# Kernel optimization log

Measured on AMD Instinct MI355X. Metric: run time of the kernel, lower is better.

The kernel has to match this reference:

```python
import jax, jax.numpy as jnp
import numpy as np
from math import ceil

B, T, FQ, D = 2, 48, 100, 512
H, DFF, L, WSZ = 8, 2048, 6, 8


def setup_inputs() -> dict:
    key = jax.random.key(0)
    ks = jax.random.split(key, 8)
    g = lambda k, shape: jax.random.normal(k, shape, jnp.float32) * 0.02
    return {
        "frame_queries": jax.random.normal(ks[0], (B, T, FQ, D), jnp.float32),
        "Wp": g(ks[1], (D, D)), "bp": jnp.zeros((D,), jnp.float32),
        "Wqkv": g(ks[2], (L, 3 * D, D)), "bqkv": jnp.zeros((L, 3 * D), jnp.float32),
        "Wo": g(ks[3], (L, D, D)), "bo": jnp.zeros((L, D), jnp.float32),
        "ln1_s": jnp.ones((L, D), jnp.float32), "ln1_b": jnp.zeros((L, D), jnp.float32),
        "W1": g(ks[4], (L, DFF, D)), "b1": jnp.zeros((L, DFF), jnp.float32),
        "W2": g(ks[5], (L, D, DFF)), "b2": jnp.zeros((L, D), jnp.float32),
        "ln2_s": jnp.ones((L, D), jnp.float32), "ln2_b": jnp.zeros((L, D), jnp.float32),
    }


def _ln(x, s, b, eps=1e-5):
    mu = x.mean(-1, keepdims=True)
    var = ((x - mu) ** 2).mean(-1, keepdims=True)
    return (x - mu) * jax.lax.rsqrt(var + eps) * s + b


def _mha(x, Wqkv_i, bqkv_i, Wo_i, bo_i, add_mask):
    # x: [Bw, S, C]; add_mask: None or [Bw, 1, S, S] additive float
    Bw, S, C = x.shape
    hd = C // H
    qkv = x @ Wqkv_i.T + bqkv_i
    q, k, v = jnp.split(qkv, 3, axis=-1)
    q = q.reshape(Bw, S, H, hd).transpose(0, 2, 1, 3)
    k = k.reshape(Bw, S, H, hd).transpose(0, 2, 1, 3)
    v = v.reshape(Bw, S, H, hd).transpose(0, 2, 1, 3)
    scores = jnp.einsum('bhqd,bhkd->bhqk', q, k) * jnp.float32(1.0 / np.sqrt(hd))
    if add_mask is not None:
        scores = scores + add_mask
    a = jax.nn.softmax(scores, axis=-1)
    o = jnp.einsum('bhqk,bhkd->bhqd', a, v).transpose(0, 2, 1, 3).reshape(Bw, S, C)
    return o @ Wo_i.T + bo_i


def _shift_mask():
    # padding mask is all-False (T % WSZ == 0), faithful construction of the
    # shifted-window additive mask as in the torch code.
    Nw = T // WSZ
    half = int(ceil(WSZ / 2))
    S = WSZ * FQ
    am = jnp.zeros((B, T), dtype=bool)
    r = jnp.roll(am, half, axis=1).reshape(B, Nw, WSZ)
    m = jnp.broadcast_to(r[..., None], (B, Nw, WSZ, WSZ))
    m = m.at[:, 0].set(m[:, 0] | m[:, 0].swapaxes(-1, -2))
    m = m.at[:, -1].set(m[:, -1] | m[:, -1].swapaxes(-1, -2))
    m = m.at[:, 0, :half, half:].set(True)
    m = m.at[:, 0, half:, :half].set(True)
    mfull = jnp.broadcast_to(m.reshape(B * Nw, WSZ, 1, WSZ, 1),
                             (B * Nw, WSZ, FQ, WSZ, FQ)).reshape(B * Nw, S, S)
    return (mfull.astype(jnp.float32) * -1000.0)[:, None]  # [B*Nw,1,S,S]


def reference(frame_queries, Wp, bp, Wqkv, bqkv, Wo, bo, ln1_s, ln1_b,
              W1, b1, W2, b2, ln2_s, ln2_b):
    Nw = T // WSZ
    half = int(ceil(WSZ / 2))
    S = WSZ * FQ
    x = frame_queries @ Wp.T + bp  # [B, T, FQ, D]
    shift_add = _shift_mask()
    for i in range(L):
        if i % 2 == 0:
            # plain window attention
            xw = x.reshape(B * Nw, S, D)
            xw = _ln(xw + _mha(xw, Wqkv[i], bqkv[i], Wo[i], bo[i], None),
                     ln1_s[i], ln1_b[i])
            x = xw.reshape(B, T, FQ, D)
        else:
            # shifted window attention
            xs = jnp.roll(x, half, axis=1)
            xw = xs.reshape(B * Nw, S, D)
            xw = _ln(xw + _mha(xw, Wqkv[i], bqkv[i], Wo[i], bo[i], shift_add),
                     ln1_s[i], ln1_b[i])
            x = jnp.roll(xw.reshape(B, T, FQ, D), -half, axis=1)
        # FFN (pointwise over channel dim)
        h = jax.nn.relu(x @ W1[i].T + b1[i]) @ W2[i].T + b2[i]
        x = _ln(x + h, ln2_s[i], ln2_b[i])
    return x  # [B, T, FQ, D] == 'lb t nq c'
```

## Files before the change

### kernel.cpp

```cpp
#include <hip/hip_runtime.h>


typedef float  f4    __attribute__((ext_vector_type(4)));
typedef __bf16 bf8   __attribute__((ext_vector_type(8)));
typedef unsigned short u16x8 __attribute__((ext_vector_type(8)));
typedef unsigned short u16x4 __attribute__((ext_vector_type(4)));

__device__ __forceinline__ unsigned short f2bf(float f) {
    unsigned int u = __builtin_bit_cast(unsigned int, f);
    u += 0x7fffu + ((u >> 16) & 1u);
    return (unsigned short)(u >> 16);
}
__device__ __forceinline__ float bf2f(unsigned short s) {
    return __builtin_bit_cast(float, ((unsigned int)s) << 16);
}

#define GLD16(gp, lp) __builtin_amdgcn_global_load_lds( \
    (const __attribute__((address_space(1))) void*)(gp), \
    (__attribute__((address_space(3))) void*)(lp), 16, 0, 0)

__device__ __forceinline__ int map_row(int r, int rshift) {
    if (!rshift) return r;
    int bb = r / 4800, rem = r % 4800;
    int tt = rem / 100, f = rem - tt * 100;
    return bb * 4800 + ((tt + rshift) % 48) * 100 + f;
}

template<int BM>
__global__ __launch_bounds__(256) void mfma_gemm(
    const unsigned short* __restrict__ A, const unsigned short* __restrict__ W,
    const float* __restrict__ bias, float* Cf, unsigned short* Cb,
    int M, int N, int K, int relu, int rshift, int qscale, int NB)
{
    constexpr int MI      = BM / 32;
    constexpr int ABUF    = BM * 32;
    constexpr int SB      = ABUF + 4096;
    constexpr int AROUNDS = BM / 64;
    __shared__ unsigned short Ls[3 * SB];
    const int tid = threadIdx.x, lane = tid & 63, wave = tid >> 6;

    const int per = gridDim.x >> 3;
    const int l = (blockIdx.x & 7) * per + (blockIdx.x >> 3);
    const int MB = M / BM;
    if (l >= NB * MB) return;
    const int n0 = (l % NB) * 128, m0 = (l / NB) * BM;

    const unsigned short* ga[AROUNDS];
    #pragma unroll
    for (int it = 0; it < AROUNDS; ++it) {
        int s = it * 256 + tid, row = s >> 2, cg = (s & 3) ^ ((row >> 1) & 3);
        ga[it] = A + (size_t)map_row(m0 + row, rshift) * K + cg * 8;
    }
    const unsigned short* gb[2];
    #pragma unroll
    for (int it = 0; it < 2; ++it) {
        int s = it * 256 + tid, row = s >> 2, cg = (s & 3) ^ ((row >> 1) & 3);
        gb[it] = W + (size_t)(n0 + row) * K + cg * 8;
    }

    const int wm = (wave >> 1) * (BM / 2), wn = (wave & 1) * 64;
    const int lr = lane & 15, quad = lane >> 4;

    auto STAGE = [&](int kt2, int buf) {
        const int k1 = kt2 << 5;
        unsigned short* Lb = &Ls[buf * SB];
        #pragma unroll
        for (int it = 0; it < AROUNDS; ++it)
            GLD16(ga[it] + k1, &Lb[(it * 256 + wave * 64) * 8]);
        #pragma unroll
        for (int it = 0; it < 2; ++it)
            GLD16(gb[it] + k1, &Lb[ABUF + (it * 256 + wave * 64) * 8]);
    };

    f4 acc[MI][4];
    #pragma unroll
    for (int i = 0; i < MI; ++i)
        #pragma unroll
        for (int j = 0; j < 4; ++j) acc[i][j] = 0.f;

    const int NK = K >> 5;
    STAGE(0, 0);
    STAGE(1, 1);

    int cb = 0;
    for (int kt = 0; kt < NK; ++kt) {
        if (kt + 1 < NK) {
            if constexpr (BM == 128) asm volatile("s_waitcnt vmcnt(4)" ::: "memory");
            else                     asm volatile("s_waitcnt vmcnt(3)" ::: "memory");
        } else {
            asm volatile("s_waitcnt vmcnt(0)" ::: "memory");
        }
        __builtin_amdgcn_s_barrier();
        __builtin_amdgcn_sched_barrier(0);
        const int ib = (cb == 0) ? 2 : cb - 1;
        if (kt + 2 < NK) STAGE(kt + 2, ib);

        const unsigned short* Ab = &Ls[cb * SB];
        const unsigned short* Bb = &Ls[cb * SB + ABUF];
        bf8 af[MI], bfr[4];
        #pragma unroll
        for (int mi = 0; mi < MI; ++mi) {
            int m = wm + mi * 16 + lr;
            int c = quad ^ ((m >> 1) & 3);
            af[mi] = __builtin_bit_cast(bf8, *(const u16x8*)&Ab[(m * 4 + c) * 8]);
        }
        #pragma unroll
        for (int ni = 0; ni < 4; ++ni) {
            int n = wn + ni * 16 + lr;
            int c = quad ^ ((n >> 1) & 3);
            bfr[ni] = __builtin_bit_cast(bf8, *(const u16x8*)&Bb[(n * 4 + c) * 8]);
        }
        #pragma unroll
        for (int mi = 0; mi < MI; ++mi)
            #pragma unroll
            for (int ni = 0; ni < 4; ++ni)
                acc[mi][ni] = __builtin_amdgcn_mfma_f32_16x16x32_bf16(
                    af[mi], bfr[ni], acc[mi][ni], 0, 0, 0);
        __builtin_amdgcn_sched_barrier(0);
        cb = (cb + 1 == 3) ? 0 : cb + 1;
    }

    #pragma unroll
    for (int mi = 0; mi < MI; ++mi) {
        #pragma unroll
        for (int ni = 0; ni < 4; ++ni) {
            const int rowg = m0 + wm + mi * 16 + quad * 4;
            const int colg = n0 + wn + ni * 16 + lr;
            const float bv = bias[colg];
            const float sc = (qscale && colg < 512) ? 0.125f : 1.0f;
            #pragma unroll
            for (int r = 0; r < 4; ++r) {
                float v = (acc[mi][ni][r] + bv) * sc;
                if (relu) v = fmaxf(v, 0.f);
                const size_t off = (size_t)(rowg + r) * N + colg;
                if (Cf) Cf[off] = v;
                if (Cb) Cb[off] = f2bf(v);
            }
        }
    }
}

template<int BM>
__global__ __launch_bounds__(256) void gemm_bk64(
    const unsigned short* __restrict__ A, const unsigned short* __restrict__ W,
    const float* __restrict__ bias, float* Cf, unsigned short* Cb,
    int M, int N, int K, int relu, int rshift, int qscale)
{
    constexpr int MI      = BM / 32;
    constexpr int ABUF    = BM * 64;
    constexpr int AROUNDS = BM / 32;
    __shared__ unsigned short As[2 * ABUF];
    __shared__ unsigned short Bs[2 * 8192];
    const int tid = threadIdx.x, lane = tid & 63, wave = tid >> 6;
    const int n0 = blockIdx.x * 128, m0 = blockIdx.y * BM;

    const unsigned short* ga[AROUNDS];
    unsigned short* la[AROUNDS];
    #pragma unroll
    for (int it = 0; it < AROUNDS; ++it) {
        int s = it * 256 + tid, row = s >> 3, cg = (s & 7) ^ (row & 7);
        ga[it] = A + (size_t)map_row(m0 + row, rshift) * K + cg * 8;
        la[it] = &As[(it * 256 + wave * 64) * 8];
    }
    const unsigned short* gb[4];
    unsigned short* lb[4];
    #pragma unroll
    for (int it = 0; it < 4; ++it) {
        int s = it * 256 + tid, row = s >> 3, cg = (s & 7) ^ (row & 7);
        gb[it] = W + (size_t)(n0 + row) * K + cg * 8;
        lb[it] = &Bs[(it * 256 + wave * 64) * 8];
    }

    const int wm = (wave >> 1) * (BM / 2), wn = (wave & 1) * 64;
    const int lr = lane & 15, quad = lane >> 4;

    f4 acc[MI][4];
    #pragma unroll
    for (int i = 0; i < MI; ++i)
        #pragma unroll
        for (int j = 0; j < 4; ++j) acc[i][j] = 0.f;

    #pragma unroll
    for (int it = 0; it < AROUNDS; ++it) GLD16(ga[it], la[it]);
    #pragma unroll
    for (int it = 0; it < 4; ++it) GLD16(gb[it], lb[it]);

    const int NK = K >> 6;
    for (int kt = 0; kt < NK; ++kt) {
        const int cb = kt & 1, nb = cb ^ 1;
        __syncthreads();
        if (kt + 1 < NK) {
            const int k1 = (kt + 1) << 6;
            #pragma unroll
            for (int it = 0; it < AROUNDS; ++it) GLD16(ga[it] + k1, la[it] + nb * ABUF);
            #pragma unroll
            for (int it = 0; it < 4; ++it)       GLD16(gb[it] + k1, lb[it] + nb * 8192);
        }
        const unsigned short* Ab = &As[cb * ABUF];
        const unsigned short* Bb = &Bs[cb * 8192];
        #pragma unroll
        for (int kh = 0; kh < 2; ++kh) {
            bf8 af[MI], bfr[4];
            #pragma unroll
            for (int mi = 0; mi < MI; ++mi) {
                int m = wm + mi * 16 + lr;
                int c = (kh * 4 + quad) ^ (m & 7);
                af[mi] = __builtin_bit_cast(bf8, *(const u16x8*)&Ab[(m * 8 + c) * 8]);
            }
            #pragma unroll
            for (int ni = 0; ni < 4; ++ni) {
                int n = wn + ni * 16 + lr;
                int c = (kh * 4 + quad) ^ (n & 7);
                bfr[ni] = __builtin_bit_cast(bf8, *(const u16x8*)&Bb[(n * 8 + c) * 8]);
            }
            #pragma unroll
            for (int mi = 0; mi < MI; ++mi)
                #pragma unroll
                for (int ni = 0; ni < 4; ++ni)
                    acc[mi][ni] = __builtin_amdgcn_mfma_f32_16x16x32_bf16(
                        af[mi], bfr[ni], acc[mi][ni], 0, 0, 0);
        }
    }

    #pragma unroll
    for (int mi = 0; mi < MI; ++mi) {
        #pragma unroll
        for (int ni = 0; ni < 4; ++ni) {
            const int rowg = m0 + wm + mi * 16 + quad * 4;
            const int colg = n0 + wn + ni * 16 + lr;
            const float bv = bias[colg];
            const float sc = (qscale && colg < 512) ? 0.125f : 1.0f;
            #pragma unroll
            for (int r = 0; r < 4; ++r) {
                float v = (acc[mi][ni][r] + bv) * sc;
                if (relu) v = fmaxf(v, 0.f);
                const size_t off = (size_t)(rowg + r) * N + colg;
                if (Cf) Cf[off] = v;
                if (Cb) Cb[off] = f2bf(v);
            }
        }
    }
}

__global__ __launch_bounds__(320) void flash_attn_mfma(
    const unsigned short* __restrict__ qkv, unsigned short* __restrict__ o,
    int masked)
{
    __shared__ unsigned short Ks[2][2048];
    __shared__ unsigned short VT[2][64 * 34];
    __shared__ unsigned short Ps[5][576];

    const int bid = blockIdx.x;
    const int h = bid & 7, kk2 = bid >> 3;
    const int qt = kk2 % 10, w = kk2 / 10;
    const int tid = threadIdx.x, lane = tid & 63, wave = tid >> 6;
    const int lr = lane & 15, quad = lane >> 4;
    const int qb = qt * 80 + wave * 16;
    const size_t wbase = (size_t)w * 800 * 1536;
    const bool do_mask = masked && ((w % 6) == 0);

    bf8 aQ[2];
    {
        const unsigned short* qp =
            qkv + wbase + (size_t)(qb + lr) * 1536 + h * 64 + quad * 8;
        aQ[0] = __builtin_bit_cast(bf8, *(const u16x8*)qp);
        aQ[1] = __builtin_bit_cast(bf8, *(const u16x8*)(qp + 32));
    }

    const unsigned short* gk = qkv;
    int kw = 0;
    if (wave < 4) {
        int s = wave * 64 + lane, row = s >> 3, clog = (s & 7) ^ (row & 7);
        gk = qkv + wbase + (size_t)row * 1536 + 512 + h * 64 + clog * 8;
        kw = wave * 512;
    }
    const int vkey = tid >> 3, vd0 = (tid & 7) * 8;
    const unsigned short* gv =
        qkv + wbase + (size_t)vkey * 1536 + 1024 + h * 64 + vd0;

    float lsum = 0.f;
    f4 oacc[4];
    #pragma unroll
    for (int dt = 0; dt < 4; ++dt) oacc[dt] = 0.f;

    const bool qhl = (qb + lr) >= 400;

    if (wave < 4) GLD16(gk, &Ks[0][kw]);
    if (tid < 256) {
        u16x8 vv0 = *(const u16x8*)gv;
        #pragma unroll
        for (int j = 0; j < 8; ++j) VT[0][(vd0 + j) * 34 + vkey] = vv0[j];
    }

    for (int kt = 0; kt < 25; ++kt) {
        const int cb = kt & 1, nb = cb ^ 1;
        const int k0 = kt * 32;
        __syncthreads();

        u16x8 vv;
        const bool pf = (kt < 24);
        if (pf && wave < 4) GLD16(gk + (size_t)(k0 + 32) * 1536, &Ks[nb][kw]);
        if (pf && tid < 256) vv = *(const u16x8*)(gv + (size_t)(k0 + 32) * 1536);

        f4 st[2];
        st[0] = 0.f; st[1] = 0.f;
        __builtin_amdgcn_s_setprio(1);
        #pragma unroll
        for (int kh = 0; kh < 2; ++kh) {
            const int cx = (kh * 4 + quad) ^ (lane & 7);
            bf8 kf0 = __builtin_bit_cast(bf8, *(const u16x8*)&Ks[cb][(lr * 8 + cx) * 8]);
            bf8 kf1 = __builtin_bit_cast(bf8, *(const u16x8*)&Ks[cb][((16 + lr) * 8 + cx) * 8]);
            st[0] = __builtin_amdgcn_mfma_f32_16x16x32_bf16(kf0, aQ[kh], st[0], 0, 0, 0);
            st[1] = __builtin_amdgcn_mfma_f32_16x16x32_bf16(kf1, aQ[kh], st[1], 0, 0, 0);
        }
        __builtin_amdgcn_s_setprio(0);

        {
            u16x4 pk0, pk1;
            float ls = 0.f;
            #pragma unroll
            for (int r = 0; r < 4; ++r) {
                float a = st[0][r], b = st[1][r];
                if (do_mask) {
                    if (((k0 + quad * 4 + r) >= 400) != qhl)      a -= 1000.f;
                    if (((k0 + 16 + quad * 4 + r) >= 400) != qhl) b -= 1000.f;
                }
                float p0 = __expf(fminf(a, 80.f));
                float p1 = __expf(fminf(b, 80.f));
                ls += p0 + p1;
                pk0[r] = (unsigned short)(__builtin_bit_cast(unsigned int, p0) >> 16);
                pk1[r] = (unsigned short)(__builtin_bit_cast(unsigned int, p1) >> 16);
            }
            lsum += ls;
            *(u16x4*)&Ps[wave][lr * 36 + quad * 4]      = pk0;
            *(u16x4*)&Ps[wave][lr * 36 + 16 + quad * 4] = pk1;
        }

        if (pf && tid < 256) {
            #pragma unroll
            for (int j = 0; j < 8; ++j) VT[nb][(vd0 + j) * 34 + vkey] = vv[j];
        }

        bf8 aP = __builtin_bit_cast(bf8, *(const u16x8*)&Ps[wave][lr * 36 + quad * 8]);
        __builtin_amdgcn_s_setprio(1);
        #pragma unroll
        for (int dt = 0; dt < 4; ++dt) {
            bf8 bV = __builtin_bit_cast(bf8,
                *(const u16x8*)&VT[cb][(dt * 16 + lr) * 34 + quad * 8]);
            oacc[dt] = __builtin_amdgcn_mfma_f32_16x16x32_bf16(aP, bV, oacc[dt], 0, 0, 0);
        }
        __builtin_amdgcn_s_setprio(0);
    }

    {
        float l = lsum;
        l += __shfl_xor(l, 16);
        l += __shfl_xor(l, 32);
        float inv[4];
        #pragma unroll
        for (int r = 0; r < 4; ++r)
            inv[r] = 1.0f / __shfl(l, quad * 4 + r);
        #pragma unroll
        for (int dt = 0; dt < 4; ++dt)
            #pragma unroll
            for (int r = 0; r < 4; ++r)
                o[((size_t)w * 800 + qb + quad * 4 + r) * 512 + h * 64 + dt * 16 + lr] =
                    f2bf(oacc[dt][r] * inv[r]);
    }
}

__global__ __launch_bounds__(256) void add_ln_kernel(
    const unsigned short* xb, const unsigned short* dlt,
    const float* __restrict__ s, const float* __restrict__ b,
    float* outf, unsigned short* outb, int rshift)
{
    const int wave = threadIdx.x >> 6, lane = threadIdx.x & 63;
    const int row = blockIdx.x * 4 + wave;
    const int xrow = map_row(row, rshift);
    const int c = lane * 8;
    u16x8 xv = *(const u16x8*)(xb  + (size_t)xrow * 512 + c);
    u16x8 dv = *(const u16x8*)(dlt + (size_t)row  * 512 + c);
    f4 u0, u1;
    #pragma unroll
    for (int j = 0; j < 4; ++j) {
        u0[j] = bf2f(xv[j])     + bf2f(dv[j]);
        u1[j] = bf2f(xv[4 + j]) + bf2f(dv[4 + j]);
    }
    float sum = u0[0]+u0[1]+u0[2]+u0[3] + u1[0]+u1[1]+u1[2]+u1[3];
    #pragma unroll
    for (int o2 = 1; o2 < 64; o2 <<= 1) sum += __shfl_xor(sum, o2);
    const float mu = sum * (1.0f / 512.0f);
    f4 d0 = u0 - mu, d1 = u1 - mu;
    float sq = d0[0]*d0[0]+d0[1]*d0[1]+d0[2]*d0[2]+d0[3]*d0[3]
             + d1[0]*d1[0]+d1[1]*d1[1]+d1[2]*d1[2]+d1[3]*d1[3];
    #pragma unroll
    for (int o2 = 1; o2 < 64; o2 <<= 1) sq += __shfl_xor(sq, o2);
    const float rs = rsqrtf(sq * (1.0f / 512.0f) + 1e-5f);
    f4 s0 = *(const f4*)(s + c), s1 = *(const f4*)(s + c + 4);
    f4 b0 = *(const f4*)(b + c), b1 = *(const f4*)(b + c + 4);
    f4 y0, y1;
    #pragma unroll
    for (int j = 0; j < 4; ++j) { y0[j] = d0[j]*rs*s0[j]+b0[j]; y1[j] = d1[j]*rs*s1[j]+b1[j]; }
    u16x8 ob;
    #pragma unroll
    for (int j = 0; j < 4; ++j) { ob[j] = f2bf(y0[j]); ob[4+j] = f2bf(y1[j]); }
    *(u16x8*)(outb + (size_t)xrow * 512 + c) = ob;
    if (outf) {
        float* of = outf + (size_t)xrow * 512 + c;
        *(f4*)of = y0; *(f4*)(of + 4) = y1;
    }
}

__global__ __launch_bounds__(256) void cast_f2b_kernel(
    const float* __restrict__ in, unsigned short* __restrict__ out, int n4)
{
    const int i = blockIdx.x * 256 + threadIdx.x;
    if (i >= n4) return;
    f4 v = ((const f4*)in)[i];
    u16x4 o4 = {f2bf(v[0]), f2bf(v[1]), f2bf(v[2]), f2bf(v[3])};
    ((u16x4*)out)[i] = o4;
}

extern "C" void kernel_launch(void* const* d_in, const int* in_sizes, int n_in,
                              void* d_out, int out_size, void* d_ws, size_t ws_size,
                              hipStream_t stream)
{
    const float* fq   = (const float*)d_in[0];
    const float* Wp   = (const float*)d_in[1];
    const float* bp   = (const float*)d_in[2];
    const float* Wqkv = (const float*)d_in[3];
    const float* bqkv = (const float*)d_in[4];
    const float* Wo   = (const float*)d_in[5];
    const float* bo   = (const float*)d_in[6];
    const float* l1s  = (const float*)d_in[7];
    const float* l1b  = (const float*)d_in[8];
    const float* W1   = (const float*)d_in[9];
    const float* b1   = (const float*)d_in[10];
    const float* W2   = (const float*)d_in[11];
    const float* b2   = (const float*)d_in[12];
    const float* l2s  = (const float*)d_in[13];
    const float* l2b  = (const float*)d_in[14];
    float* out = (float*)d_out;

    unsigned short* xb   = (unsigned short*)d_ws;
    unsigned short* qkvb = xb + 4915200;
    unsigned short* hbuf = qkvb + 14745600;
    unsigned short* wbuf = hbuf + 19660800;
    unsigned short* obuf = hbuf;
    unsigned short* t1b  = qkvb;
    unsigned short* fqb  = hbuf;
    unsigned short* wqA = wbuf;
    unsigned short* woA = wqA + 4718592;
    unsigned short* w1A = woA + 1572864;
    unsigned short* w2A = w1A + 6291456;
    unsigned short* wpA = w2A + 6291456;

    const dim3 blk(256);
    #define G8(n) dim3((((n) + 7) & ~7))
    cast_f2b_kernel<<<dim3(4800), blk, 0, stream>>>(fq,   fqb, 1228800);
    cast_f2b_kernel<<<dim3(4608), blk, 0, stream>>>(Wqkv, wqA, 1179648);
    cast_f2b_kernel<<<dim3(1536), blk, 0, stream>>>(Wo,   woA, 393216);
    cast_f2b_kernel<<<dim3(6144), blk, 0, stream>>>(W1,   w1A, 1572864);
    cast_f2b_kernel<<<dim3(6144), blk, 0, stream>>>(W2,   w2A, 1572864);
    cast_f2b_kernel<<<dim3(256),  blk, 0, stream>>>(Wp,   wpA, 65536);
    mfma_gemm<64><<<G8(600), blk, 0, stream>>>(fqb, wpA, bp, nullptr, xb,
                                               9600, 512, 512, 0, 0, 0, 4);

    for (int i = 0; i < 6; ++i) {
        const int rsh = (i & 1) ? 44 : 0;
        const unsigned short* wq = wqA + (size_t)i * 786432;
        const unsigned short* wo = woA + (size_t)i * 262144;
        const unsigned short* w1 = w1A + (size_t)i * 1048576;
        const unsigned short* w2 = w2A + (size_t)i * 1048576;
        mfma_gemm<128><<<G8(900), blk, 0, stream>>>(xb, wq, bqkv + i * 1536,
                                                    nullptr, qkvb, 9600, 1536, 512, 0, rsh, 1, 12);
        flash_attn_mfma<<<dim3(960), dim3(320), 0, stream>>>(qkvb, obuf, i & 1);
        mfma_gemm<64><<<G8(600), blk, 0, stream>>>(obuf, wo, bo + i * 512,
                                                   nullptr, t1b, 9600, 512, 512, 0, 0, 0, 4);
        add_ln_kernel<<<dim3(2400), blk, 0, stream>>>(xb, t1b, l1s + i * 512, l1b + i * 512,
                                                      nullptr, xb, rsh);
        gemm_bk64<128><<<dim3(16, 75), blk, 0, stream>>>(xb, w1, b1 + i * 2048,
                                                         nullptr, hbuf, 9600, 2048, 512, 1, 0, 0);
        gemm_bk64<64><<<dim3(4, 150), blk, 0, stream>>>(hbuf, w2, b2 + i * 512,
                                                        nullptr, t1b, 9600, 512, 2048, 0, 0, 0);
        add_ln_kernel<<<dim3(2400), blk, 0, stream>>>(xb, t1b, l2s + i * 512, l2b + i * 512,
                                                      (i == 5) ? out : nullptr, xb, 0);
    }
    #undef G8
}
```

Baseline: 1.191 ms.

## Load V tiles via async global-to-LDS and transpose with ds_read_b64_tr_b16

Replaces the register-staged V load and scalar transposed LDS stores with direct global_load_lds copies into a permuted layout. The B operand is then read with the hardware transposing LDS read instruction. This removes per-element 2-byte LDS stores and the register round trip on the V path, so the V prefetch overlaps with compute the same way K does. It relies on a hand-derived key/dim permutation and inline asm with an explicit waitcnt, which limits compiler scheduling and is fragile if the layout mapping is wrong.

```diff
diff --git a/kernel.cpp b/kernel.cpp
--- a/kernel.cpp
+++ b/kernel.cpp
@@ -5,6 +5,8 @@
 typedef __bf16 bf8   __attribute__((ext_vector_type(8)));
 typedef unsigned short u16x8 __attribute__((ext_vector_type(8)));
 typedef unsigned short u16x4 __attribute__((ext_vector_type(4)));
+typedef unsigned int   u32x2 __attribute__((ext_vector_type(2)));
+typedef unsigned int   u32x4 __attribute__((ext_vector_type(4)));
 
 __device__ __forceinline__ unsigned short f2bf(float f) {
     unsigned int u = __builtin_bit_cast(unsigned int, f);
@@ -247,7 +249,7 @@
     int masked)
 {
     __shared__ unsigned short Ks[2][2048];
-    __shared__ unsigned short VT[2][64 * 34];
+    __shared__ __align__(16) unsigned short VTs[2][2048];
     __shared__ unsigned short Ps[5][576];
 
     const int bid = blockIdx.x;
@@ -274,9 +276,19 @@
         gk = qkv + wbase + (size_t)row * 1536 + 512 + h * 64 + clog * 8;
         kw = wave * 512;
     }
-    const int vkey = tid >> 3, vd0 = (tid & 7) * 8;
-    const unsigned short* gv =
-        qkv + wbase + (size_t)vkey * 1536 + 1024 + h * 64 + vd0;
+    const unsigned short* gvp = qkv;
+    if (wave < 4) {
+        int c = wave * 64 + lane, S = c >> 3, wc = c & 7;
+        int vkey = 8 * (S & 3) + 4 * ((S >> 2) & 1) + (wc >> 1);
+        int vdim = 16 * (S >> 3) + 8 * (wc & 1);
+        gvp = qkv + wbase + (size_t)vkey * 1536 + 1024 + h * 64 + vdim;
+    }
+
+    unsigned vtb;
+    {
+        auto p3 = (__attribute__((address_space(3))) unsigned short*)&VTs[0][0];
+        vtb = (unsigned)(unsigned long long)p3 + (unsigned)(lane << 3);
+    }
 
     float lsum = 0.f;
     f4 oacc[4];
@@ -285,11 +297,9 @@
 
     const bool qhl = (qb + lr) >= 400;
 
-    if (wave < 4) GLD16(gk, &Ks[0][kw]);
-    if (tid < 256) {
-        u16x8 vv0 = *(const u16x8*)gv;
-        #pragma unroll
-        for (int j = 0; j < 8; ++j) VT[0][(vd0 + j) * 34 + vkey] = vv0[j];
+    if (wave < 4) {
+        GLD16(gk, &Ks[0][kw]);
+        GLD16(gvp, &VTs[0][wave * 512]);
     }
 
     for (int kt = 0; kt < 25; ++kt) {
@@ -297,10 +307,11 @@
         const int k0 = kt * 32;
         __syncthreads();
 
-        u16x8 vv;
         const bool pf = (kt < 24);
-        if (pf && wave < 4) GLD16(gk + (size_t)(k0 + 32) * 1536, &Ks[nb][kw]);
-        if (pf && tid < 256) vv = *(const u16x8*)(gv + (size_t)(k0 + 32) * 1536);
+        if (pf && wave < 4) {
+            GLD16(gk  + (size_t)(k0 + 32) * 1536, &Ks[nb][kw]);
+            GLD16(gvp + (size_t)(k0 + 32) * 1536, &VTs[nb][wave * 512]);
+        }
 
         f4 st[2];
         st[0] = 0.f; st[1] = 0.f;
@@ -336,18 +347,29 @@
             *(u16x4*)&Ps[wave][lr * 36 + 16 + quad * 4] = pk1;
         }
 
-        if (pf && tid < 256) {
-            #pragma unroll
-            for (int j = 0; j < 8; ++j) VT[nb][(vd0 + j) * 34 + vkey] = vv[j];
-        }
-
         bf8 aP = __builtin_bit_cast(bf8, *(const u16x8*)&Ps[wave][lr * 36 + quad * 8]);
+        const unsigned va = vtb + ((unsigned)cb << 12);
+        u32x2 t0, t1, t2, t3, t4, t5, t6, t7;
+        asm volatile("ds_read_b64_tr_b16 %0, %1"             : "=v"(t0) : "v"(va));
+        asm volatile("ds_read_b64_tr_b16 %0, %1 offset:512"  : "=v"(t1) : "v"(va));
+        asm volatile("ds_read_b64_tr_b16 %0, %1 offset:1024" : "=v"(t2) : "v"(va));
+        asm volatile("ds_read_b64_tr_b16 %0, %1 offset:1536" : "=v"(t3) : "v"(va));
+        asm volatile("ds_read_b64_tr_b16 %0, %1 offset:2048" : "=v"(t4) : "v"(va));
+        asm volatile("ds_read_b64_tr_b16 %0, %1 offset:2560" : "=v"(t5) : "v"(va));
+        asm volatile("ds_read_b64_tr_b16 %0, %1 offset:3072" : "=v"(t6) : "v"(va));
+        asm volatile("ds_read_b64_tr_b16 %0, %1 offset:3584" : "=v"(t7) : "v"(va));
+        asm volatile("s_waitcnt lgkmcnt(0)" ::: "memory");
+        __builtin_amdgcn_sched_barrier(0);
         __builtin_amdgcn_s_setprio(1);
-        #pragma unroll
-        for (int dt = 0; dt < 4; ++dt) {
-            bf8 bV = __builtin_bit_cast(bf8,
-                *(const u16x8*)&VT[cb][(dt * 16 + lr) * 34 + quad * 8]);
-            oacc[dt] = __builtin_amdgcn_mfma_f32_16x16x32_bf16(aP, bV, oacc[dt], 0, 0, 0);
+        {
+            u32x4 b0 = {t0[0], t0[1], t1[0], t1[1]};
+            u32x4 b1 = {t2[0], t2[1], t3[0], t3[1]};
+            u32x4 b2 = {t4[0], t4[1], t5[0], t5[1]};
+            u32x4 b3 = {t6[0], t6[1], t7[0], t7[1]};
+            oacc[0] = __builtin_amdgcn_mfma_f32_16x16x32_bf16(aP, __builtin_bit_cast(bf8, b0), oacc[0], 0, 0, 0);
+            oacc[1] = __builtin_amdgcn_mfma_f32_16x16x32_bf16(aP, __builtin_bit_cast(bf8, b1), oacc[1], 0, 0, 0);
+            oacc[2] = __builtin_amdgcn_mfma_f32_16x16x32_bf16(aP, __builtin_bit_cast(bf8, b2), oacc[2], 0, 0, 0);
+            oacc[3] = __builtin_amdgcn_mfma_f32_16x16x32_bf16(aP, __builtin_bit_cast(bf8, b3), oacc[3], 0, 0, 0);
         }
         __builtin_amdgcn_s_setprio(0);
     }
```

Result: faster. 1.159 ms (-2.7%).
